# Performance work log

Measured on AMD Instinct MI355X. Metric: run time of the kernel, lower is better.

Reference implementation:

```python
import jax, jax.numpy as jnp
import numpy as np

VOCAB = 50257
N_EMBD = 640
BLOCK = 256
B = 16


def setup_inputs() -> dict:
    key = jax.random.key(0)
    ks = jax.random.split(key, 8)
    std = 0.02
    return {
        "idx": jax.random.randint(ks[0], (B, BLOCK), 0, VOCAB, dtype=jnp.int64 if jax.config.jax_enable_x64 else jnp.int32),
        "w_embed": jax.random.normal(ks[1], (VOCAB, N_EMBD), jnp.float32) * std,
        "w_pos": jax.random.normal(ks[2], (BLOCK, N_EMBD), jnp.float32) * std,
        "wq": jax.random.normal(ks[3], (N_EMBD, N_EMBD), jnp.float32) * std,
        "wk": jax.random.normal(ks[4], (N_EMBD, N_EMBD), jnp.float32) * std,
        "wv": jax.random.normal(ks[5], (N_EMBD, N_EMBD), jnp.float32) * std,
        "w_out": jax.random.normal(ks[6], (VOCAB, N_EMBD), jnp.float32) * std,
        "b_out": jnp.zeros((VOCAB,), jnp.float32),
    }


def reference(idx, w_embed, w_pos, wq, wk, wv, w_out, b_out):
    # idx: (B, T) token ids. Dropout is identity (eval mode).
    Bt, T = idx.shape
    x = w_embed[idx] + w_pos[:T]                      # (B, T, D)
    q = jnp.einsum('btd,ed->bte', x, wq)              # torch Linear: x @ W.T
    k = jnp.einsum('btd,ed->bte', x, wk)
    v = jnp.einsum('btd,ed->bte', x, wv)
    scale = jnp.asarray(N_EMBD ** 0.5, x.dtype)
    scores = jnp.einsum('btd,bsd->bts', q, k) / scale  # (B, T, T)
    causal = jnp.triu(jnp.ones((T, T), bool), k=1)     # True above diagonal
    scores = jnp.where(causal, jnp.asarray(-jnp.inf, scores.dtype), scores)
    attn = jax.nn.softmax(scores, axis=-1)
    attn_out = jnp.einsum('bts,bsd->btd', attn, v)     # (B, T, D)
    logits = jnp.einsum('btd,vd->btv', attn_out, w_out) + b_out  # (B, T, V)
    return logits
```

## Files before the change

kernel.cpp:

```cpp
#include <hip/hip_runtime.h>
#include <hip/hip_bf16.h>
#include <stdint.h>

#define VOCAB 50257
#define VPAD  50432
#define DIM   640
#define SEQ   256
#define NBATCH 16
#define MROWS 4096

using bf16 = __hip_bfloat16;
typedef __attribute__((ext_vector_type(8))) short short8;
typedef __attribute__((ext_vector_type(4))) float f32x4;
struct bf16x4 { bf16 a, b, c, d; };

__device__ __forceinline__ void gld_lds16(const void* g, void* l) {
  __builtin_amdgcn_global_load_lds(
      (const __attribute__((address_space(1))) void*)g,
      (__attribute__((address_space(3))) void*)l, 16, 0, 0);
}

#define BAR() asm volatile("s_barrier" ::: "memory")
#define VMC0() asm volatile("s_waitcnt vmcnt(0)" ::: "memory")

__global__ void embed_kernel(const int* __restrict__ idx,
                             const float* __restrict__ we,
                             const float* __restrict__ wp,
                             bf16* __restrict__ xb) {
  int row = blockIdx.x;
  int t = row & (SEQ - 1);
  int tok = idx[row];
  const float* src = we + (long)tok * DIM;
  const float* pos = wp + (long)t * DIM;
  for (int d = threadIdx.x * 4; d < DIM; d += blockDim.x * 4) {
    float4 s = *(const float4*)(src + d);
    float4 p = *(const float4*)(pos + d);
    bf16x4 o = { __float2bfloat16(s.x + p.x), __float2bfloat16(s.y + p.y),
                 __float2bfloat16(s.z + p.z), __float2bfloat16(s.w + p.w) };
    *(bf16x4*)(xb + (long)row * DIM + d) = o;
  }
}

__global__ void conv4_kernel(const float* __restrict__ src, bf16* __restrict__ dst,
                             long n_src, long n_dst) {
  long i = ((long)blockIdx.x * blockDim.x + threadIdx.x) * 4;
  long stride = (long)gridDim.x * blockDim.x * 4;
  for (; i < n_dst; i += stride) {
    float4 v = (i < n_src) ? *(const float4*)(src + i) : make_float4(0.f, 0.f, 0.f, 0.f);
    bf16x4 o = { __float2bfloat16(v.x), __float2bfloat16(v.y),
                 __float2bfloat16(v.z), __float2bfloat16(v.w) };
    *(bf16x4*)(dst + i) = o;
  }
}

__global__ void transpose_v(const bf16* __restrict__ v, bf16* __restrict__ vt) {
  long i = (long)blockIdx.x * blockDim.x + threadIdx.x;
  if (i >= (long)NBATCH * DIM * SEQ) return;
  int t = (int)(i & (SEQ - 1));
  long be = i >> 8;
  int e = (int)(be % DIM);
  int b = (int)(be / DIM);
  vt[i] = v[((long)b * SEQ + t) * DIM + e];
}

__global__ void softmax_kernel(const float* __restrict__ sc, bf16* __restrict__ p) {
  int wid = threadIdx.x >> 6, lane = threadIdx.x & 63;
  int row = blockIdx.x * 4 + wid;
  int t = row & (SEQ - 1);
  const float* srow = sc + (long)row * SEQ;
  const float rsc = 0.03952847075210474f;
  float v[4];
  float mx = -1e30f;
#pragma unroll
  for (int i = 0; i < 4; ++i) {
    int s = lane + 64 * i;
    v[i] = (s <= t) ? srow[s] * rsc : -1e30f;
    mx = fmaxf(mx, v[i]);
  }
#pragma unroll
  for (int off = 32; off; off >>= 1) mx = fmaxf(mx, __shfl_xor(mx, off, 64));
  float sum = 0.f;
#pragma unroll
  for (int i = 0; i < 4; ++i) {
    int s = lane + 64 * i;
    v[i] = (s <= t) ? __expf(v[i] - mx) : 0.f;
    sum += v[i];
  }
#pragma unroll
  for (int off = 32; off; off >>= 1) sum += __shfl_xor(sum, off, 64);
  float inv = 1.f / sum;
#pragma unroll
  for (int i = 0; i < 4; ++i)
    p[(long)row * SEQ + lane + 64 * i] = __float2bfloat16(v[i] * inv);
}

template <int NT, typename OUT_T, bool BIAS>
__global__ __launch_bounds__(256, 4) void gemm_pipe(
    const bf16* __restrict__ Ag, const bf16* __restrict__ Bg,
    OUT_T* __restrict__ Cg, const float* __restrict__ bias,
    int K, int ldc, int Nstore, long sA, long sB, long sC) {
  __shared__ __align__(16) char lds[32768];
  const int tid = threadIdx.x;
  const int lane = tid & 63, wv = tid >> 6;
  const int lr = lane & 15, h16 = lane >> 4;

  const int tm = blockIdx.x, tn = blockIdx.y, bz = blockIdx.z;
  const bf16* A = Ag + (long)bz * sA + (long)tm * 128 * K;
  const bf16* B = Bg + (long)bz * sB + (long)tn * 128 * K;

  int srcE[2], dstW[2];
#pragma unroll
  for (int j = 0; j < 2; ++j) {
    int d = j * 256 + tid;
    int b = d ^ ((d >> 3) & 3);
    srcE[j] = (b >> 2) * K + (b & 3) * 8;
    dstW[j] = (j * 256 + wv * 64) * 16;
  }
  const bf16* aS0 = A + srcE[0];
  const bf16* aS1 = A + srcE[1];
  const bf16* bS0 = B + srcE[0];
  const bf16* bS1 = B + srcE[1];
  auto STAGE = [&](int slot, int t) {
    int kOff = t * 32;
    gld_lds16(aS0 + kOff, lds + slot + dstW[0]);
    gld_lds16(aS1 + kOff, lds + slot + dstW[1]);
    gld_lds16(bS0 + kOff, lds + slot + 8192 + dstW[0]);
    gld_lds16(bS1 + kOff, lds + slot + 8192 + dstW[1]);
  };

  const int wr = (wv >> 1) * 64, wc = (wv & 1) * 64;
  int aoff[4], boff[4];
#pragma unroll
  for (int m = 0; m < 4; ++m) {
    int La = (wr + m * 16 + lr) * 64 + h16 * 16;
    aoff[m] = La ^ (((La >> 7) & 3) << 4);
    int Lb = (wc + m * 16 + lr) * 64 + h16 * 16;
    boff[m] = 8192 + (Lb ^ (((Lb >> 7) & 3) << 4));
  }

  f32x4 acc[4][4] = {};
  short8 a[4], b[4];

  STAGE(0, 0);
  VMC0();
  BAR();

#pragma unroll 2
  for (int t = 0; t < NT; ++t) {
    const int cur = (t & 1) * 16384;
    if (t + 1 < NT) STAGE(16384 - cur, t + 1);
#pragma unroll
    for (int m = 0; m < 4; ++m) a[m] = *(const short8*)(lds + cur + aoff[m]);
#pragma unroll
    for (int n = 0; n < 4; ++n) b[n] = *(const short8*)(lds + cur + boff[n]);
    __builtin_amdgcn_s_setprio(1);
#pragma unroll
    for (int m = 0; m < 4; ++m)
#pragma unroll
      for (int n = 0; n < 4; ++n)
        acc[m][n] = __builtin_amdgcn_mfma_f32_16x16x32_bf16(a[m], b[n], acc[m][n], 0, 0, 0);
    __builtin_amdgcn_s_setprio(0);
    if (t + 1 < NT) VMC0();
    BAR();
  }

  if constexpr (sizeof(OUT_T) == 4) {
    float* Cf = (float*)Cg + (long)bz * sC;
    float bv[4];
#pragma unroll
    for (int n = 0; n < 4; ++n) {
      int col = tn * 128 + wc + lr + n * 16;
      bv[n] = (BIAS && col < Nstore) ? bias[col] : 0.f;
    }
    char* reg = lds + wv * 8192;
    const int rowL = lane & 31, cb = lane >> 5;
#pragma unroll
    for (int mm = 0; mm < 2; ++mm) {
#pragma unroll
      for (int mp = 0; mp < 2; ++mp)
#pragma unroll
        for (int n = 0; n < 4; ++n) {
          f32x4 v = acc[mm * 2 + mp][n];
          v[0] += bv[n]; v[1] += bv[n]; v[2] += bv[n]; v[3] += bv[n];
          int col = lr + n * 16;
          int rho = mp * 16 + h16 * 4;
          int w = col * 32 + (rho ^ ((col & 7) << 2));
          *(f32x4*)(reg + w * 4) = v;
        }
      const long rowg = tm * 128 + wr + mm * 32 + rowL;
#pragma unroll
      for (int k = 0; k < 8; ++k) {
        f32x4 o;
#pragma unroll
        for (int c = 0; c < 4; ++c) {
          int col = k * 8 + cb * 4 + c;
          int w = col * 32 + (rowL ^ ((col & 7) << 2));
          o[c] = *(const float*)(reg + w * 4);
        }
        int gcol = tn * 128 + wc + k * 8 + cb * 4;
        float* dst = Cf + rowg * (long)ldc + gcol;
        if (gcol + 3 < Nstore) {
          *(f32x4*)dst = o;
        } else {
#pragma unroll
          for (int c = 0; c < 4; ++c)
            if (gcol + c < Nstore) dst[c] = o[c];
        }
      }
    }
  } else {
    OUT_T* C = Cg + (long)bz * sC;
    const int crow0 = tm * 128 + wr + h16 * 4;
    const int ccol0 = tn * 128 + wc + lr;
#pragma unroll
    for (int m = 0; m < 4; ++m)
#pragma unroll
      for (int n = 0; n < 4; ++n) {
        int col = ccol0 + n * 16;
        if (col < Nstore) {
#pragma unroll
          for (int j = 0; j < 4; ++j) {
            long row = crow0 + m * 16 + j;
            C[row * ldc + col] = __float2bfloat16(acc[m][n][j]);
          }
        }
      }
  }
}

__global__ __launch_bounds__(512, 6) void gemm8(
    const bf16* __restrict__ Ag, const bf16* __restrict__ Bg,
    float* __restrict__ Cg, const float* __restrict__ bias) {
  __shared__ __align__(16) char lds[32768];
  const int tid = threadIdx.x;
  const int lane = tid & 63, wv = tid >> 6;
  const int lr = lane & 15, h16 = lane >> 4;

  const int tm = blockIdx.x, tn = blockIdx.y;
  const bf16* A = Ag + (long)tm * 128 * DIM;
  const bf16* B = Bg + (long)tn * 128 * DIM;

  int srcE, dstW;
  {
    int d = tid;
    int b = d ^ ((d >> 3) & 3);
    srcE = (b >> 2) * DIM + (b & 3) * 8;
    dstW = (wv * 64) * 16;
  }
  const bf16* aS = A + srcE;
  const bf16* bS = B + srcE;
  auto STAGE = [&](int slot, int t) {
    int kOff = t * 32;
    gld_lds16(aS + kOff, lds + slot + dstW);
    gld_lds16(bS + kOff, lds + slot + 8192 + dstW);
  };

  const int wr = (wv >> 2) * 64, wc = (wv & 3) * 32;
  int aoff[4], boff[2];
#pragma unroll
  for (int m = 0; m < 4; ++m) {
    int La = (wr + m * 16 + lr) * 64 + h16 * 16;
    aoff[m] = La ^ (((La >> 7) & 3) << 4);
  }
#pragma unroll
  for (int n = 0; n < 2; ++n) {
    int Lb = (wc + n * 16 + lr) * 64 + h16 * 16;
    boff[n] = 8192 + (Lb ^ (((Lb >> 7) & 3) << 4));
  }

  f32x4 acc[4][2] = {};
  short8 a[4], b[2];

  STAGE(0, 0);
  VMC0();
  BAR();

#pragma unroll 2
  for (int t = 0; t < 20; ++t) {
    const int cur = (t & 1) * 16384;
    if (t + 1 < 20) STAGE(16384 - cur, t + 1);
#pragma unroll
    for (int m = 0; m < 4; ++m) a[m] = *(const short8*)(lds + cur + aoff[m]);
#pragma unroll
    for (int n = 0; n < 2; ++n) b[n] = *(const short8*)(lds + cur + boff[n]);
    __builtin_amdgcn_s_setprio(1);
#pragma unroll
    for (int m = 0; m < 4; ++m)
#pragma unroll
      for (int n = 0; n < 2; ++n)
        acc[m][n] = __builtin_amdgcn_mfma_f32_16x16x32_bf16(a[m], b[n], acc[m][n], 0, 0, 0);
    __builtin_amdgcn_s_setprio(0);
    if (t + 1 < 20) VMC0();
    BAR();
  }

  const int crow0 = tm * 128 + wr + h16 * 4;
  const int ccol0 = tn * 128 + wc + lr;
  float bv[2];
#pragma unroll
  for (int n = 0; n < 2; ++n) {
    int col = ccol0 + n * 16;
    bv[n] = (col < VOCAB) ? bias[col] : 0.f;
  }
#pragma unroll
  for (int m = 0; m < 4; ++m)
#pragma unroll
    for (int n = 0; n < 2; ++n) {
      int col = ccol0 + n * 16;
      if (col < VOCAB) {
#pragma unroll
        for (int j = 0; j < 4; ++j)
          Cg[(long)(crow0 + m * 16 + j) * VOCAB + col] = acc[m][n][j] + bv[n];
      }
    }
}

extern "C" void kernel_launch(void* const* d_in, const int* in_sizes, int n_in,
                              void* d_out, int out_size, void* d_ws, size_t ws_size,
                              hipStream_t stream) {
  const int*   idx     = (const int*)d_in[0];
  const float* w_embed = (const float*)d_in[1];
  const float* w_pos   = (const float*)d_in[2];
  const float* wq      = (const float*)d_in[3];
  const float* wk      = (const float*)d_in[4];
  const float* wv      = (const float*)d_in[5];
  const float* w_out   = (const float*)d_in[6];
  const float* b_out   = (const float*)d_in[7];
  float* out = (float*)d_out;

  size_t off = 0;
  auto alloc = [&](size_t bytes) {
    void* p = (char*)d_ws + off;
    off += (bytes + 255) & ~(size_t)255;
    return p;
  };
  bf16* x_bf    = (bf16*)alloc((size_t)MROWS * DIM * 2);
  bf16* wqkv_bf = (bf16*)alloc((size_t)3 * DIM * DIM * 2);
  bf16* wout_bf = (bf16*)alloc((size_t)VPAD * DIM * 2);
  bf16* qkv     = (bf16*)alloc((size_t)3 * MROWS * DIM * 2);
  bf16* vT      = (bf16*)alloc((size_t)NBATCH * DIM * SEQ * 2);
  float* scores = (float*)alloc((size_t)NBATCH * SEQ * SEQ * 4);
  bf16* P       = (bf16*)alloc((size_t)NBATCH * SEQ * SEQ * 2);
  bf16* attn    = (bf16*)alloc((size_t)MROWS * DIM * 2);

  const long QKV_S = (long)MROWS * DIM;
  const long W_S   = (long)DIM * DIM;

  embed_kernel<<<MROWS, 256, 0, stream>>>(idx, w_embed, w_pos, x_bf);

  conv4_kernel<<<256, 256, 0, stream>>>(wq, wqkv_bf,           W_S, W_S);
  conv4_kernel<<<256, 256, 0, stream>>>(wk, wqkv_bf + W_S,     W_S, W_S);
  conv4_kernel<<<256, 256, 0, stream>>>(wv, wqkv_bf + 2 * W_S, W_S, W_S);
  conv4_kernel<<<2048, 256, 0, stream>>>(w_out, wout_bf, (long)VOCAB * DIM, (long)VPAD * DIM);

  gemm_pipe<20, bf16, false><<<dim3(MROWS / 128, DIM / 128, 3), 256, 0, stream>>>(
      x_bf, wqkv_bf, qkv, nullptr, DIM, DIM, DIM, 0, W_S, QKV_S);

  {
    long n = (long)NBATCH * DIM * SEQ;
    transpose_v<<<(int)((n + 255) / 256), 256, 0, stream>>>(qkv + 2 * QKV_S, vT);
  }

  gemm_pipe<20, float, false><<<dim3(SEQ / 128, SEQ / 128, NBATCH), 256, 0, stream>>>(
      qkv, qkv + QKV_S, scores, nullptr, DIM, SEQ, SEQ,
      (long)SEQ * DIM, (long)SEQ * DIM, (long)SEQ * SEQ);

  softmax_kernel<<<MROWS / 4, 256, 0, stream>>>(scores, P);

  gemm_pipe<8, bf16, false><<<dim3(SEQ / 128, DIM / 128, NBATCH), 256, 0, stream>>>(
      P, vT, attn, nullptr, SEQ, DIM, DIM,
      (long)SEQ * SEQ, (long)DIM * SEQ, (long)SEQ * DIM);

  gemm8<<<dim3(MROWS / 128, VPAD / 128), 512, 0, stream>>>(attn, wout_bf, out, b_out);
}
```

Measured before the change: 604.8 us.

## Fuse V transpose into projection epilogue and add causal-skipping 64-tile scores kernel

The V projection now writes its output directly in transposed (b, e, t) layout from the GEMM epilogue, which removes the separate transpose_v kernel and its scattered memory traffic. The QK^T scores GEMM is replaced by a 64x64-tiled kernel that skips tiles entirely above the causal diagonal and launches more blocks for better occupancy. In exchange, the transposed epilogue stores are strided and uncoalesced, and the V projection becomes a separate launch. Scores above the diagonal stay unwritten, which is fine because softmax masks them.

```diff
diff --git a/kernel.cpp b/kernel.cpp
--- a/kernel.cpp
+++ b/kernel.cpp
@@ -53,16 +53,6 @@
   }
 }
 
-__global__ void transpose_v(const bf16* __restrict__ v, bf16* __restrict__ vt) {
-  long i = (long)blockIdx.x * blockDim.x + threadIdx.x;
-  if (i >= (long)NBATCH * DIM * SEQ) return;
-  int t = (int)(i & (SEQ - 1));
-  long be = i >> 8;
-  int e = (int)(be % DIM);
-  int b = (int)(be / DIM);
-  vt[i] = v[((long)b * SEQ + t) * DIM + e];
-}
-
 __global__ void softmax_kernel(const float* __restrict__ sc, bf16* __restrict__ p) {
   int wid = threadIdx.x >> 6, lane = threadIdx.x & 63;
   int row = blockIdx.x * 4 + wid;
@@ -94,7 +84,7 @@
     p[(long)row * SEQ + lane + 64 * i] = __float2bfloat16(v[i] * inv);
 }
 
-template <int NT, typename OUT_T, bool BIAS>
+template <int NT, typename OUT_T, bool BIAS, bool TRV>
 __global__ __launch_bounds__(256, 4) void gemm_pipe(
     const bf16* __restrict__ Ag, const bf16* __restrict__ Bg,
     OUT_T* __restrict__ Cg, const float* __restrict__ bias,
@@ -221,11 +211,90 @@
 #pragma unroll
           for (int j = 0; j < 4; ++j) {
             long row = crow0 + m * 16 + j;
-            C[row * ldc + col] = __float2bfloat16(acc[m][n][j]);
+            if constexpr (TRV) {
+              C[((long)(row >> 8) * DIM + col) * SEQ + (row & 255)] =
+                  __float2bfloat16(acc[m][n][j]);
+            } else {
+              C[row * ldc + col] = __float2bfloat16(acc[m][n][j]);
+            }
           }
         }
       }
   }
+}
+
+__global__ __launch_bounds__(256, 6) void scores64(
+    const bf16* __restrict__ qg, const bf16* __restrict__ kg,
+    float* __restrict__ sc) {
+  const int tm = blockIdx.x, tn = blockIdx.y, bz = blockIdx.z;
+  if (tn > tm) return;
+  __shared__ __align__(16) char lds[16384];
+  const int tid = threadIdx.x;
+  const int lane = tid & 63, wv = tid >> 6;
+  const int lr = lane & 15, h16 = lane >> 4;
+
+  const bf16* A = qg + (long)bz * SEQ * DIM + (long)tm * 64 * DIM;
+  const bf16* B = kg + (long)bz * SEQ * DIM + (long)tn * 64 * DIM;
+
+  int srcE, dstW;
+  {
+    int d = tid;
+    int b = d ^ ((d >> 3) & 3);
+    srcE = (b >> 2) * DIM + (b & 3) * 8;
+    dstW = (wv * 64) * 16;
+  }
+  auto STAGE = [&](int slot, int t) {
+    int kOff = t * 32;
+    gld_lds16(A + srcE + kOff, lds + slot + dstW);
+    gld_lds16(B + srcE + kOff, lds + slot + 4096 + dstW);
+  };
+
+  const int wm = wv >> 1, wn = wv & 1;
+  int aoff[2], boff[2];
+#pragma unroll
+  for (int m = 0; m < 2; ++m) {
+    int La = (wm * 32 + m * 16 + lr) * 64 + h16 * 16;
+    aoff[m] = La ^ (((La >> 7) & 3) << 4);
+    int Lb = (wn * 32 + m * 16 + lr) * 64 + h16 * 16;
+    boff[m] = 4096 + (Lb ^ (((Lb >> 7) & 3) << 4));
+  }
+
+  f32x4 acc[2][2] = {};
+  short8 a[2], b[2];
+
+  STAGE(0, 0);
+  VMC0();
+  BAR();
+
+#pragma unroll 2
+  for (int t = 0; t < 20; ++t) {
+    const int cur = (t & 1) * 8192;
+    if (t + 1 < 20) STAGE(8192 - cur, t + 1);
+#pragma unroll
+    for (int m = 0; m < 2; ++m) a[m] = *(const short8*)(lds + cur + aoff[m]);
+#pragma unroll
+    for (int n = 0; n < 2; ++n) b[n] = *(const short8*)(lds + cur + boff[n]);
+    __builtin_amdgcn_s_setprio(1);
+#pragma unroll
+    for (int m = 0; m < 2; ++m)
+#pragma unroll
+      for (int n = 0; n < 2; ++n)
+        acc[m][n] = __builtin_amdgcn_mfma_f32_16x16x32_bf16(a[m], b[n], acc[m][n], 0, 0, 0);
+    __builtin_amdgcn_s_setprio(0);
+    if (t + 1 < 20) VMC0();
+    BAR();
+  }
+
+  float* S = sc + (long)bz * SEQ * SEQ;
+  const int crow0 = tm * 64 + wm * 32 + h16 * 4;
+  const int ccol0 = tn * 64 + wn * 32 + lr;
+#pragma unroll
+  for (int m = 0; m < 2; ++m)
+#pragma unroll
+    for (int n = 0; n < 2; ++n)
+#pragma unroll
+      for (int j = 0; j < 4; ++j)
+        S[(long)(crow0 + m * 16 + j) * SEQ + ccol0 + n * 16] = acc[m][n][j];
 }
 
 __global__ __launch_bounds__(512, 6) void gemm8(
@@ -337,7 +406,7 @@
   bf16* x_bf    = (bf16*)alloc((size_t)MROWS * DIM * 2);
   bf16* wqkv_bf = (bf16*)alloc((size_t)3 * DIM * DIM * 2);
   bf16* wout_bf = (bf16*)alloc((size_t)VPAD * DIM * 2);
-  bf16* qkv     = (bf16*)alloc((size_t)3 * MROWS * DIM * 2);
+  bf16* qkv     = (bf16*)alloc((size_t)2 * MROWS * DIM * 2);
   bf16* vT      = (bf16*)alloc((size_t)NBATCH * DIM * SEQ * 2);
   float* scores = (float*)alloc((size_t)NBATCH * SEQ * SEQ * 4);
   bf16* P       = (bf16*)alloc((size_t)NBATCH * SEQ * SEQ * 2);
@@ -353,21 +422,17 @@
   conv4_kernel<<<256, 256, 0, stream>>>(wv, wqkv_bf + 2 * W_S, W_S, W_S);
   conv4_kernel<<<2048, 256, 0, stream>>>(w_out, wout_bf, (long)VOCAB * DIM, (long)VPAD * DIM);
 
-  gemm_pipe<20, bf16, false><<<dim3(MROWS / 128, DIM / 128, 3), 256, 0, stream>>>(
+  gemm_pipe<20, bf16, false, false><<<dim3(MROWS / 128, DIM / 128, 2), 256, 0, stream>>>(
       x_bf, wqkv_bf, qkv, nullptr, DIM, DIM, DIM, 0, W_S, QKV_S);
 
-  {
-    long n = (long)NBATCH * DIM * SEQ;
-    transpose_v<<<(int)((n + 255) / 256), 256, 0, stream>>>(qkv + 2 * QKV_S, vT);
-  }
-
-  gemm_pipe<20, float, false><<<dim3(SEQ / 128, SEQ / 128, NBATCH), 256, 0, stream>>>(
-      qkv, qkv + QKV_S, scores, nullptr, DIM, SEQ, SEQ,
-      (long)SEQ * DIM, (long)SEQ * DIM, (long)SEQ * SEQ);
+  gemm_pipe<20, bf16, false, true><<<dim3(MROWS / 128, DIM / 128, 1), 256, 0, stream>>>(
+      x_bf, wqkv_bf + 2 * W_S, vT, nullptr, DIM, DIM, DIM, 0, 0, 0);
+
+  scores64<<<dim3(4, 4, NBATCH), 256, 0, stream>>>(qkv, qkv + QKV_S, scores);
 
   softmax_kernel<<<MROWS / 4, 256, 0, stream>>>(scores, P);
 
-  gemm_pipe<8, bf16, false><<<dim3(SEQ / 128, DIM / 128, NBATCH), 256, 0, stream>>>(
+  gemm_pipe<8, bf16, false, false><<<dim3(SEQ / 128, DIM / 128, NBATCH), 256, 0, stream>>>(
       P, vT, attn, nullptr, SEQ, DIM, DIM,
       (long)SEQ * SEQ, (long)DIM * SEQ, (long)SEQ * DIM);
 
```

After: 600.2 us, median of 3. No clear change (-0.8%).
